# Kernel optimization log

Hardware: AMD Instinct MI355X
Metric: run time of the kernel (lower is better)

The kernel has to match this reference:

```python
import jax, jax.numpy as jnp
import numpy as np

N_NODES = 50000
SEQ_LEN = 32
N_TOKENS = 100000
EMB_DIM = 128          # in_feats / 2
IN_FEATS = 256
N_HIDDEN = 256
N_CLASSES = 40
N_EDGES = 800000
PAD_IX = 0


def setup_inputs() -> dict:
    key = jax.random.key(0)
    k1, k2, k3, k4, k5, k6 = jax.random.split(key, 6)
    features = jax.random.randint(k1, (N_NODES, SEQ_LEN), 0, N_TOKENS, dtype=jnp.int32)
    src = jax.random.randint(k2, (N_EDGES,), 0, N_NODES, dtype=jnp.int32)
    dst = jax.random.randint(k3, (N_EDGES,), 0, N_NODES, dtype=jnp.int32)
    emb_table = jax.random.normal(k4, (N_TOKENS, EMB_DIM), dtype=jnp.float32) * 0.02
    W1 = jax.random.normal(k5, (IN_FEATS, N_HIDDEN), dtype=jnp.float32) * 0.02
    b1 = jnp.zeros((N_HIDDEN,), dtype=jnp.float32)
    W2 = jax.random.normal(k6, (N_HIDDEN, N_CLASSES), dtype=jnp.float32) * 0.02
    b2 = jnp.zeros((N_CLASSES,), dtype=jnp.float32)
    return {"features": features, "src": src, "dst": dst,
            "emb_table": emb_table, "W1": W1, "b1": b1, "W2": W2, "b2": b2}


def _apply_embs(features, emb_table):
    # padding_idx row contributes zeros (nn.Embedding padding_idx semantics)
    emb = emb_table.at[PAD_IX].set(0.0)
    h = emb[features]                                    # [N, L, D]
    seq_len = jnp.sum(features != PAD_IX, axis=1)        # [N]
    seq_len = jnp.maximum(seq_len, 1)[:, None].astype(h.dtype)
    h1 = h.sum(axis=1) / seq_len                         # masked mean
    h2 = h.max(axis=1)                                   # max pool (pads are 0)
    return jnp.concatenate((h1, h2), axis=1)             # [N, 2D]


def _graph_conv(h, src, dst, norm_s, norm_d, W, b):
    # DGL GraphConv, norm='both': out = D_in^{-1/2} A D_out^{-1/2} h W + b
    hw = h @ W                                           # transform first (smaller msgs)
    m = (hw * norm_s[:, None])[src]                      # gather messages [E, F]
    agg = jax.ops.segment_sum(m, dst, num_segments=N_NODES)
    return agg * norm_d[:, None] + b


def reference(features, src, dst, emb_table, W1, b1, W2, b2):
    ones_e = jnp.ones((src.shape[0],), dtype=jnp.float32)
    deg_out = jnp.maximum(jax.ops.segment_sum(ones_e, src, num_segments=N_NODES), 1.0)
    deg_in = jnp.maximum(jax.ops.segment_sum(ones_e, dst, num_segments=N_NODES), 1.0)
    norm_s = deg_out ** -0.5
    norm_d = deg_in ** -0.5

    h = _apply_embs(features, emb_table)                 # [N, in_feats]
    h = jax.nn.relu(_graph_conv(h, src, dst, norm_s, norm_d, W1, b1))
    # dropout is identity in eval mode
    h = _graph_conv(h, src, dst, norm_s, norm_d, W2, b2)
    return h                                             # [N, n_classes]
```

## Files before the change

### kernel.cpp

```cpp
#include <hip/hip_runtime.h>
#include <math.h>

#define N_NODES 50000
#define SEQ_LEN 32
#define EMB_DIM 128
#define IN_FEATS 256
#define N_HIDDEN 256
#define N_CLASSES 40
#define N_EDGES 800000
#define N_TOKENS 100000

#define SLOT 64
#define NBIN 196
#define BINCAP 4608
#define EPB 4000

typedef short short8 __attribute__((ext_vector_type(8)));
typedef float f32x4 __attribute__((ext_vector_type(4)));

__device__ __forceinline__ unsigned short f2bf(float x) {
  unsigned int u = __float_as_uint(x);
  unsigned int r = (u + 0x7FFFu + ((u >> 16) & 1u)) >> 16;
  return (unsigned short)r;
}
__device__ __forceinline__ float bf2f(unsigned short s) {
  return __uint_as_float((unsigned int)s << 16);
}
__device__ __forceinline__ unsigned int pack2bf(float a, float b) {
  return (unsigned int)f2bf(a) | ((unsigned int)f2bf(b) << 16);
}

__global__ __launch_bounds__(256) void k_pre(const int* __restrict__ src,
                                             const int* __restrict__ dst,
                                             int* __restrict__ gcntD,
                                             int* __restrict__ gcntS,
                                             unsigned int* __restrict__ dbin,
                                             unsigned char* __restrict__ sbin,
                                             const float* __restrict__ emb,
                                             unsigned short* __restrict__ emb_b,
                                             const float* __restrict__ W1,
                                             unsigned short* __restrict__ Wp1,
                                             const float* __restrict__ W2,
                                             unsigned short* __restrict__ Wp2) {
  __shared__ int cntD[NBIN], cntS[NBIN], baseD[NBIN], baseS[NBIN];
  int b = blockIdx.x, tid = threadIdx.x;
  if (b < 200) {
    if (tid < NBIN) { cntD[tid] = 0; cntS[tid] = 0; }
    __syncthreads();
    int e0 = b * EPB;
    for (int j = tid; j < EPB; j += 256) {
      int d = dst[e0 + j], s = src[e0 + j];
      atomicAdd(&cntD[d >> 8], 1);
      atomicAdd(&cntS[s >> 8], 1);
    }
    __syncthreads();
    if (tid < NBIN) {
      baseD[tid] = atomicAdd(&gcntD[tid], cntD[tid]);
      baseS[tid] = atomicAdd(&gcntS[tid], cntS[tid]);
      cntD[tid] = 0;
      cntS[tid] = 0;
    }
    __syncthreads();
    for (int j = tid; j < EPB; j += 256) {
      int d = dst[e0 + j], s = src[e0 + j];
      int bd = d >> 8, bs = s >> 8;
      int od = atomicAdd(&cntD[bd], 1);
      int pd = baseD[bd] + od;
      if (pd < BINCAP) dbin[(size_t)bd * BINCAP + pd] = ((unsigned int)s << 8) | (unsigned int)(d & 255);
      int os = atomicAdd(&cntS[bs], 1);
      int ps = baseS[bs] + os;
      if (ps < BINCAP) sbin[(size_t)bs * BINCAP + ps] = (unsigned char)(s & 255);
    }
  } else if (b < 200 + 2048) {
    const int total = N_TOKENS * EMB_DIM / 4;
    for (int i = (b - 200) * 256 + tid; i < total; i += 2048 * 256) {
      float4 v = ((const float4*)emb)[i];
      ushort4 o;
      o.x = f2bf(v.x); o.y = f2bf(v.y); o.z = f2bf(v.z); o.w = f2bf(v.w);
      ((ushort4*)emb_b)[i] = o;
    }
  } else if (b < 200 + 2048 + 32) {
    int g = (b - 2248) * 256 + tid;
    int lane = g & 63, jb = (g >> 6) & 15, kt = g >> 10;
    int col = jb * 16 + (lane & 15);
    int kbase = kt * 32 + (lane >> 4) * 8;
    unsigned short* o = Wp1 + (size_t)g * 8;
    #pragma unroll
    for (int e = 0; e < 8; ++e) o[e] = f2bf(W1[(size_t)(kbase + e) * N_HIDDEN + col]);
  } else {
    int g = (b - 2280) * 256 + tid;
    if (g < 8 * 3 * 64) {
      int lane = g & 63, jb = (g >> 6) % 3, kt = g / (3 * 64);
      int col = jb * 16 + (lane & 15);
      int kbase = kt * 32 + (lane >> 4) * 8;
      unsigned short* o = Wp2 + (size_t)g * 8;
      #pragma unroll
      for (int e = 0; e < 8; ++e)
        o[e] = (col < N_CLASSES) ? f2bf(W2[(size_t)(kbase + e) * N_CLASSES + col]) : (unsigned short)0;
    }
  }
}

__global__ __launch_bounds__(256) void k_graph2(const unsigned int* __restrict__ dbin,
                                                const int* __restrict__ gcntD,
                                                const unsigned char* __restrict__ sbin,
                                                const int* __restrict__ gcntS,
                                                int* __restrict__ cursor,
                                                int* __restrict__ csr_pad,
                                                float* __restrict__ norm_s,
                                                float* __restrict__ norm_d) {
  __shared__ int cntD[256], cntS[256];
  int tid = threadIdx.x, b = blockIdx.x;
  cntD[tid] = 0; cntS[tid] = 0;
  __syncthreads();
  int n = min(gcntD[b], BINCAP);
  const unsigned int* bb = dbin + (size_t)b * BINCAP;
  for (int j = tid; j < n; j += 256) {
    unsigned int e = bb[j];
    int lo = e & 255;
    int slot = atomicAdd(&cntD[lo], 1);
    if (slot < SLOT) csr_pad[(size_t)(b * 256 + lo) * SLOT + slot] = (int)(e >> 8);
  }
  int ns = min(gcntS[b], BINCAP);
  const unsigned char* sb = sbin + (size_t)b * BINCAP;
  for (int j = tid; j < ns; j += 256) atomicAdd(&cntS[sb[j]], 1);
  __syncthreads();
  int node = b * 256 + tid;
  if (node < N_NODES) {
    cursor[node] = min(cntD[tid], SLOT);
    norm_d[node] = 1.0f / sqrtf((float)max(cntD[tid], 1));
    norm_s[node] = 1.0f / sqrtf((float)max(cntS[tid], 1));
  }
}

__global__ __launch_bounds__(512) void k_emb_mm1(const int* __restrict__ feats,
                                                 const uint4* __restrict__ rows4,
                                                 const unsigned short* __restrict__ Wp,
                                                 const float* __restrict__ norm_s,
                                                 unsigned short* __restrict__ out) {
  __shared__ unsigned short sA[64 * 256];
  int tid = threadIdx.x;
  int w = tid >> 6, lane = tid & 63;
  int r0 = blockIdx.x * 64;
  int lq = lane & 15, qg = lane >> 4, laneL = lane & 31;

  #pragma unroll
  for (int n = 0; n < 8; ++n) {
    int r = w * 8 + n;
    int node = r0 + r;
    int tok0 = 0;
    if (node < N_NODES) tok0 = feats[(size_t)node * SEQ_LEN + laneL];
    unsigned long long m = __ballot(tok0 != 0);
    int cnt = (int)__popcll(m & 0xFFFFFFFFull);
    float inv = 1.0f / (float)max(cnt, 1);

    float s0 = 0.f, s1 = 0.f, s2 = 0.f, s3 = 0.f, s4 = 0.f, s5 = 0.f, s6 = 0.f, s7 = 0.f;
    float m0 = 0.f, m1 = 0.f, m2 = 0.f, m3 = 0.f, m4 = 0.f, m5 = 0.f, m6 = 0.f, m7 = 0.f;
    bool first = true;
    #pragma unroll
    for (int t = 0; t < 8; ++t) {
      int tok = __shfl(tok0, t * 4 + qg);
      uint4 v = make_uint4(0u, 0u, 0u, 0u);
      if (tok) v = rows4[(size_t)tok * 16 + lq];
      float f0 = bf2f((unsigned short)(v.x & 0xFFFF)), f1 = bf2f((unsigned short)(v.x >> 16));
      float f2 = bf2f((unsigned short)(v.y & 0xFFFF)), f3 = bf2f((unsigned short)(v.y >> 16));
      float f4 = bf2f((unsigned short)(v.z & 0xFFFF)), f5 = bf2f((unsigned short)(v.z >> 16));
      float f6 = bf2f((unsigned short)(v.w & 0xFFFF)), f7 = bf2f((unsigned short)(v.w >> 16));
      s0 += f0; s1 += f1; s2 += f2; s3 += f3; s4 += f4; s5 += f5; s6 += f6; s7 += f7;
      if (first) { m0 = f0; m1 = f1; m2 = f2; m3 = f3; m4 = f4; m5 = f5; m6 = f6; m7 = f7; first = false; }
      else {
        m0 = fmaxf(m0, f0); m1 = fmaxf(m1, f1); m2 = fmaxf(m2, f2); m3 = fmaxf(m3, f3);
        m4 = fmaxf(m4, f4); m5 = fmaxf(m5, f5); m6 = fmaxf(m6, f6); m7 = fmaxf(m7, f7);
      }
    }
    #pragma unroll
    for (int mask = 16; mask <= 32; mask <<= 1) {
      s0 += __shfl_xor(s0, mask); s1 += __shfl_xor(s1, mask);
      s2 += __shfl_xor(s2, mask); s3 += __shfl_xor(s3, mask);
      s4 += __shfl_xor(s4, mask); s5 += __shfl_xor(s5, mask);
      s6 += __shfl_xor(s6, mask); s7 += __shfl_xor(s7, mask);
      m0 = fmaxf(m0, __shfl_xor(m0, mask)); m1 = fmaxf(m1, __shfl_xor(m1, mask));
      m2 = fmaxf(m2, __shfl_xor(m2, mask)); m3 = fmaxf(m3, __shfl_xor(m3, mask));
      m4 = fmaxf(m4, __shfl_xor(m4, mask)); m5 = fmaxf(m5, __shfl_xor(m5, mask));
      m6 = fmaxf(m6, __shfl_xor(m6, mask)); m7 = fmaxf(m7, __shfl_xor(m7, mask));
    }
    if (qg == 0) {
      int kb1 = lq, kb2 = 16 + lq;
      *(uint4*)&sA[r * 256 + ((kb1 ^ (r & 7)) << 3)] =
          make_uint4(pack2bf(s0 * inv, s1 * inv), pack2bf(s2 * inv, s3 * inv),
                     pack2bf(s4 * inv, s5 * inv), pack2bf(s6 * inv, s7 * inv));
      *(uint4*)&sA[r * 256 + ((kb2 ^ (r & 7)) << 3)] =
          make_uint4(pack2bf(m0, m1), pack2bf(m2, m3), pack2bf(m4, m5), pack2bf(m6, m7));
    }
  }
  __syncthreads();

  const short8* W8 = (const short8*)Wp;
  f32x4 acc[4][2];
  #pragma unroll
  for (int i = 0; i < 4; ++i) { acc[i][0] = (f32x4){0.f,0.f,0.f,0.f}; acc[i][1] = (f32x4){0.f,0.f,0.f,0.f}; }

  #pragma unroll
  for (int kt = 0; kt < 8; ++kt) {
    short8 a[4];
    int kb = kt * 4 + (lane >> 4);
    #pragma unroll
    for (int ri = 0; ri < 4; ++ri) {
      int r = ri * 16 + (lane & 15);
      a[ri] = *(const short8*)&sA[r * 256 + ((kb ^ (r & 7)) << 3)];
    }
    short8 b0 = W8[(kt * 16 + w * 2 + 0) * 64 + lane];
    short8 b1 = W8[(kt * 16 + w * 2 + 1) * 64 + lane];
    #pragma unroll
    for (int ri = 0; ri < 4; ++ri) {
      acc[ri][0] = __builtin_amdgcn_mfma_f32_16x16x32_bf16(a[ri], b0, acc[ri][0], 0, 0, 0);
      acc[ri][1] = __builtin_amdgcn_mfma_f32_16x16x32_bf16(a[ri], b1, acc[ri][1], 0, 0, 0);
    }
  }

  #pragma unroll
  for (int ri = 0; ri < 4; ++ri) {
    #pragma unroll
    for (int rr = 0; rr < 4; ++rr) {
      int row = r0 + ri * 16 + (lane >> 4) * 4 + rr;
      if (row < N_NODES) {
        float ns = norm_s[row];
        #pragma unroll
        for (int jb = 0; jb < 2; ++jb) {
          int col = w * 32 + jb * 16 + (lane & 15);
          out[(size_t)row * 256 + col] = f2bf(acc[ri][jb][rr] * ns);
        }
      }
    }
  }
}

__global__ __launch_bounds__(256) void k_agg1(const uint4* __restrict__ rows4,
                                              const int* __restrict__ cursor,
                                              const int* __restrict__ csr_pad,
                                              const float* __restrict__ norm_d,
                                              const float* __restrict__ b1,
                                              uint4* __restrict__ out4) {
  int tid = threadIdx.x;
  int w = tid >> 6, lane = tid & 63;
  int node = blockIdx.x * 4 + w;
  int cnt = __builtin_amdgcn_readfirstlane(cursor[node]);
  const int* csr = csr_pad + (size_t)node * SLOT;
  int half = lane >> 5, lq = lane & 31;

  float a0 = 0.f, a1 = 0.f, a2 = 0.f, a3 = 0.f, a4 = 0.f, a5 = 0.f, a6 = 0.f, a7 = 0.f;
  int e = 0;
  for (; e + 8 <= cnt; e += 8) {
    int s0 = csr[e + 0 + half], s1 = csr[e + 2 + half];
    int s2 = csr[e + 4 + half], s3 = csr[e + 6 + half];
    uint4 v0 = rows4[(size_t)s0 * 32 + lq];
    uint4 v1 = rows4[(size_t)s1 * 32 + lq];
    uint4 v2 = rows4[(size_t)s2 * 32 + lq];
    uint4 v3 = rows4[(size_t)s3 * 32 + lq];
    #pragma unroll
    for (int i = 0; i < 4; ++i) {
      uint4 v = (i == 0) ? v0 : (i == 1) ? v1 : (i == 2) ? v2 : v3;
      a0 += bf2f((unsigned short)(v.x & 0xFFFF)); a1 += bf2f((unsigned short)(v.x >> 16));
      a2 += bf2f((unsigned short)(v.y & 0xFFFF)); a3 += bf2f((unsigned short)(v.y >> 16));
      a4 += bf2f((unsigned short)(v.z & 0xFFFF)); a5 += bf2f((unsigned short)(v.z >> 16));
      a6 += bf2f((unsigned short)(v.w & 0xFFFF)); a7 += bf2f((unsigned short)(v.w >> 16));
    }
  }
  for (; e + 2 <= cnt; e += 2) {
    int s = csr[e + half];
    uint4 v = rows4[(size_t)s * 32 + lq];
    a0 += bf2f((unsigned short)(v.x & 0xFFFF)); a1 += bf2f((unsigned short)(v.x >> 16));
    a2 += bf2f((unsigned short)(v.y & 0xFFFF)); a3 += bf2f((unsigned short)(v.y >> 16));
    a4 += bf2f((unsigned short)(v.z & 0xFFFF)); a5 += bf2f((unsigned short)(v.z >> 16));
    a6 += bf2f((unsigned short)(v.w & 0xFFFF)); a7 += bf2f((unsigned short)(v.w >> 16));
  }
  if (e < cnt) {
    uint4 v = make_uint4(0u, 0u, 0u, 0u);
    if (half == 0) v = rows4[(size_t)csr[e] * 32 + lq];
    a0 += bf2f((unsigned short)(v.x & 0xFFFF)); a1 += bf2f((unsigned short)(v.x >> 16));
    a2 += bf2f((unsigned short)(v.y & 0xFFFF)); a3 += bf2f((unsigned short)(v.y >> 16));
    a4 += bf2f((unsigned short)(v.z & 0xFFFF)); a5 += bf2f((unsigned short)(v.z >> 16));
    a6 += bf2f((unsigned short)(v.w & 0xFFFF)); a7 += bf2f((unsigned short)(v.w >> 16));
  }
  a0 += __shfl_xor(a0, 32); a1 += __shfl_xor(a1, 32);
  a2 += __shfl_xor(a2, 32); a3 += __shfl_xor(a3, 32);
  a4 += __shfl_xor(a4, 32); a5 += __shfl_xor(a5, 32);
  a6 += __shfl_xor(a6, 32); a7 += __shfl_xor(a7, 32);

  if (half == 0) {
    float nd = norm_d[node];
    float4 bb0 = *(const float4*)&b1[8 * lq];
    float4 bb1 = *(const float4*)&b1[8 * lq + 4];
    float o0 = fmaxf(a0 * nd + bb0.x, 0.f), o1 = fmaxf(a1 * nd + bb0.y, 0.f);
    float o2 = fmaxf(a2 * nd + bb0.z, 0.f), o3 = fmaxf(a3 * nd + bb0.w, 0.f);
    float o4 = fmaxf(a4 * nd + bb1.x, 0.f), o5 = fmaxf(a5 * nd + bb1.y, 0.f);
    float o6 = fmaxf(a6 * nd + bb1.z, 0.f), o7 = fmaxf(a7 * nd + bb1.w, 0.f);
    out4[(size_t)node * 32 + lq] = make_uint4(pack2bf(o0, o1), pack2bf(o2, o3),
                                              pack2bf(o4, o5), pack2bf(o6, o7));
  }
}

__global__ __launch_bounds__(256) void k_mm2(const unsigned short* __restrict__ h2b,
                                             const unsigned short* __restrict__ Wp,
                                             const float* __restrict__ norm_s,
                                             unsigned short* __restrict__ out) {
  __shared__ unsigned short sA[64 * 256];
  int tid = threadIdx.x;
  int r0 = blockIdx.x * 64;
  #pragma unroll
  for (int it = 0; it < 8; ++it) {
    int idx = it * 256 + tid;
    int r = idx >> 5, kb = idx & 31;
    uint4 v = make_uint4(0, 0, 0, 0);
    int row = r0 + r;
    if (row < N_NODES) v = *(const uint4*)(h2b + (size_t)row * 256 + kb * 8);
    *(uint4*)&sA[r * 256 + ((kb ^ (r & 7)) << 3)] = v;
  }
  __syncthreads();

  int w = tid >> 6, lane = tid & 63;
  const short8* W8 = (const short8*)Wp;
  f32x4 acc[3];
  #pragma unroll
  for (int j = 0; j < 3; ++j) acc[j] = (f32x4){0.f, 0.f, 0.f, 0.f};

  #pragma unroll
  for (int kt = 0; kt < 8; ++kt) {
    int r = w * 16 + (lane & 15);
    int kb = kt * 4 + (lane >> 4);
    short8 a = *(const short8*)&sA[r * 256 + ((kb ^ (r & 7)) << 3)];
    #pragma unroll
    for (int jb = 0; jb < 3; ++jb) {
      short8 b = W8[(kt * 3 + jb) * 64 + lane];
      acc[jb] = __builtin_amdgcn_mfma_f32_16x16x32_bf16(a, b, acc[jb], 0, 0, 0);
    }
  }

  #pragma unroll
  for (int rr = 0; rr < 4; ++rr) {
    int row = r0 + w * 16 + (lane >> 4) * 4 + rr;
    if (row < N_NODES) {
      float ns = norm_s[row];
      #pragma unroll
      for (int jb = 0; jb < 3; ++jb) {
        int col = jb * 16 + (lane & 15);
        if (col < N_CLASSES) out[(size_t)row * N_CLASSES + col] = f2bf(acc[jb][rr] * ns);
      }
    }
  }
}

__global__ __launch_bounds__(256) void k_agg2(const uint2* __restrict__ rows2,
                                              const int* __restrict__ cursor,
                                              const int* __restrict__ csr_pad,
                                              const float* __restrict__ norm_d,
                                              const float* __restrict__ b2,
                                              float* __restrict__ out) {
  int tid = threadIdx.x;
  int w = tid >> 6, lane = tid & 63;
  int node = blockIdx.x * 4 + w;
  int slot = lane / 10, fl = lane % 10;
  int cnt = __builtin_amdgcn_readfirstlane(cursor[node]);
  const int* csr = csr_pad + (size_t)node * SLOT;

  float a0 = 0.f, a1 = 0.f, a2 = 0.f, a3 = 0.f;
  if (slot < 6) {
    for (int e = slot; e < cnt; e += 6) {
      int s = csr[e];
      uint2 v = rows2[(size_t)s * 10 + fl];
      a0 += bf2f((unsigned short)(v.x & 0xFFFF));
      a1 += bf2f((unsigned short)(v.x >> 16));
      a2 += bf2f((unsigned short)(v.y & 0xFFFF));
      a3 += bf2f((unsigned short)(v.y >> 16));
    }
  }
  float r10_0 = __shfl(a0, lane + 10), r10_1 = __shfl(a1, lane + 10), r10_2 = __shfl(a2, lane + 10), r10_3 = __shfl(a3, lane + 10);
  float r20_0 = __shfl(a0, lane + 20), r20_1 = __shfl(a1, lane + 20), r20_2 = __shfl(a2, lane + 20), r20_3 = __shfl(a3, lane + 20);
  float r30_0 = __shfl(a0, lane + 30), r30_1 = __shfl(a1, lane + 30), r30_2 = __shfl(a2, lane + 30), r30_3 = __shfl(a3, lane + 30);
  float r40_0 = __shfl(a0, lane + 40), r40_1 = __shfl(a1, lane + 40), r40_2 = __shfl(a2, lane + 40), r40_3 = __shfl(a3, lane + 40);
  float r50_0 = __shfl(a0, lane + 50), r50_1 = __shfl(a1, lane + 50), r50_2 = __shfl(a2, lane + 50), r50_3 = __shfl(a3, lane + 50);
  if (slot == 0) {
    a0 += r10_0 + r20_0 + r30_0 + r40_0 + r50_0;
    a1 += r10_1 + r20_1 + r30_1 + r40_1 + r50_1;
    a2 += r10_2 + r20_2 + r30_2 + r40_2 + r50_2;
    a3 += r10_3 + r20_3 + r30_3 + r40_3 + r50_3;
    float nd = norm_d[node];
    float4 bb = *(const float4*)&b2[4 * fl];
    float4 o = make_float4(a0 * nd + bb.x, a1 * nd + bb.y, a2 * nd + bb.z, a3 * nd + bb.w);
    *(float4*)&out[(size_t)node * N_CLASSES + 4 * fl] = o;
  }
}

extern "C" void kernel_launch(void* const* d_in, const int* in_sizes, int n_in,
                              void* d_out, int out_size, void* d_ws, size_t ws_size,
                              hipStream_t stream) {
  const int*   feats = (const int*)d_in[0];
  const int*   src   = (const int*)d_in[1];
  const int*   dst   = (const int*)d_in[2];
  const float* emb   = (const float*)d_in[3];
  const float* W1    = (const float*)d_in[4];
  const float* b1    = (const float*)d_in[5];
  const float* W2    = (const float*)d_in[6];
  const float* b2    = (const float*)d_in[7];
  float* out = (float*)d_out;

  char* base = (char*)d_ws;
  size_t off = 0;
  auto alloc = [&](size_t bytes) -> char* {
    char* p = base + off;
    off += (bytes + 255) & ~(size_t)255;
    return p;
  };
  unsigned short* hb      = (unsigned short*)alloc((size_t)N_NODES * N_HIDDEN * 2);
  unsigned short* msgb    = (unsigned short*)alloc((size_t)N_NODES * N_HIDDEN * 2);
  unsigned short* hw2b    = (unsigned short*)alloc((size_t)N_NODES * N_CLASSES * 2);
  unsigned short* emb_b   = (unsigned short*)alloc((size_t)N_TOKENS * EMB_DIM * 2);
  unsigned short* Wp1     = (unsigned short*)alloc((size_t)8 * 16 * 64 * 8 * 2);
  unsigned short* Wp2     = (unsigned short*)alloc((size_t)8 * 3 * 64 * 8 * 2);
  int*   gcnt    = (int*)alloc((size_t)512 * 4);
  int*   gcntD   = gcnt;
  int*   gcntS   = gcnt + 256;
  int*   cursor  = (int*)alloc((size_t)N_NODES * 4);
  float* norm_s  = (float*)alloc((size_t)N_NODES * 4);
  float* norm_d  = (float*)alloc((size_t)N_NODES * 4);
  unsigned int*  dbin = (unsigned int*)alloc((size_t)NBIN * BINCAP * 4);
  unsigned char* sbin = (unsigned char*)alloc((size_t)NBIN * BINCAP);
  int*   csr_pad = (int*)alloc((size_t)N_NODES * SLOT * 4);

  hipMemsetAsync(gcnt, 0, 512 * 4, stream);

  k_pre<<<200 + 2048 + 32 + 6, 256, 0, stream>>>(src, dst, gcntD, gcntS, dbin, sbin,
                                                 emb, emb_b, W1, Wp1, W2, Wp2);
  k_graph2<<<NBIN, 256, 0, stream>>>(dbin, gcntD, sbin, gcntS, cursor, csr_pad, norm_s, norm_d);

  int gemm_blocks = (N_NODES + 63) / 64;
  k_emb_mm1<<<gemm_blocks, 512, 0, stream>>>(feats, (const uint4*)emb_b, Wp1, norm_s, msgb);
  k_agg1<<<N_NODES / 4, 256, 0, stream>>>((const uint4*)msgb, cursor, csr_pad, norm_d, b1, (uint4*)hb);
  k_mm2<<<gemm_blocks, 256, 0, stream>>>(hb, Wp2, norm_s, hw2b);
  k_agg2<<<N_NODES / 4, 256, 0, stream>>>((const uint2*)hw2b, cursor, csr_pad, norm_d, b2, out);
}
```

Measured before the change: 212.3 us.

## Split embedding pooling from first GEMM and deepen aggregation unroll

Splits the fused embedding-pool plus first GEMM kernel into a standalone per-node embedding kernel writing bf16 features to global memory, and a separate 256-thread MFMA GEMM with 4x4 tiles per wave. This targets the poor latency hiding of the fused kernel, where few blocks each serially gathered embeddings for many rows. It also unrolls the first aggregation loop to 16 edges per iteration for more outstanding gathers. The cost is an extra write and read of the intermediate feature matrix plus one more launch.

```diff
diff --git a/kernel.cpp b/kernel.cpp
--- a/kernel.cpp
+++ b/kernel.cpp
@@ -29,6 +29,13 @@
 __device__ __forceinline__ unsigned int pack2bf(float a, float b) {
   return (unsigned int)f2bf(a) | ((unsigned int)f2bf(b) << 16);
 }
+
+#define ACC8(v) do { \
+  a[0] += bf2f((unsigned short)((v).x & 0xFFFF)); a[1] += bf2f((unsigned short)((v).x >> 16)); \
+  a[2] += bf2f((unsigned short)((v).y & 0xFFFF)); a[3] += bf2f((unsigned short)((v).y >> 16)); \
+  a[4] += bf2f((unsigned short)((v).z & 0xFFFF)); a[5] += bf2f((unsigned short)((v).z >> 16)); \
+  a[6] += bf2f((unsigned short)((v).w & 0xFFFF)); a[7] += bf2f((unsigned short)((v).w >> 16)); \
+} while (0)
 
 __global__ __launch_bounds__(256) void k_pre(const int* __restrict__ src,
                                              const int* __restrict__ dst,
@@ -133,89 +140,98 @@
   }
 }
 
-__global__ __launch_bounds__(512) void k_emb_mm1(const int* __restrict__ feats,
-                                                 const uint4* __restrict__ rows4,
-                                                 const unsigned short* __restrict__ Wp,
-                                                 const float* __restrict__ norm_s,
-                                                 unsigned short* __restrict__ out) {
+__global__ __launch_bounds__(256) void k_embed(const int* __restrict__ feats,
+                                               const uint4* __restrict__ rows4,
+                                               uint4* __restrict__ h4) {
+  int tid = threadIdx.x;
+  int w = tid >> 6, lane = tid & 63;
+  int node = blockIdx.x * 4 + w;
+  int lq = lane & 15, qg = lane >> 4;
+  int laneL = lane & 31;
+
+  int tok0 = feats[(size_t)node * SEQ_LEN + laneL];
+  unsigned long long m = __ballot(tok0 != 0);
+  int cnt = (int)__popcll(m & 0xFFFFFFFFull);
+  float inv = 1.0f / (float)max(cnt, 1);
+
+  float s0 = 0.f, s1 = 0.f, s2 = 0.f, s3 = 0.f, s4 = 0.f, s5 = 0.f, s6 = 0.f, s7 = 0.f;
+  float m0 = -INFINITY, m1 = -INFINITY, m2 = -INFINITY, m3 = -INFINITY;
+  float m4 = -INFINITY, m5 = -INFINITY, m6 = -INFINITY, m7 = -INFINITY;
+  #pragma unroll
+  for (int t = 0; t < 8; ++t) {
+    int tok = __shfl(tok0, t * 4 + qg);
+    uint4 v = make_uint4(0u, 0u, 0u, 0u);
+    if (tok) v = rows4[(size_t)tok * 16 + lq];
+    float f0 = bf2f((unsigned short)(v.x & 0xFFFF)), f1 = bf2f((unsigned short)(v.x >> 16));
+    float f2 = bf2f((unsigned short)(v.y & 0xFFFF)), f3 = bf2f((unsigned short)(v.y >> 16));
+    float f4 = bf2f((unsigned short)(v.z & 0xFFFF)), f5 = bf2f((unsigned short)(v.z >> 16));
+    float f6 = bf2f((unsigned short)(v.w & 0xFFFF)), f7 = bf2f((unsigned short)(v.w >> 16));
+    s0 += f0; s1 += f1; s2 += f2; s3 += f3; s4 += f4; s5 += f5; s6 += f6; s7 += f7;
+    m0 = fmaxf(m0, f0); m1 = fmaxf(m1, f1); m2 = fmaxf(m2, f2); m3 = fmaxf(m3, f3);
+    m4 = fmaxf(m4, f4); m5 = fmaxf(m5, f5); m6 = fmaxf(m6, f6); m7 = fmaxf(m7, f7);
+  }
+  #pragma unroll
+  for (int mask = 16; mask <= 32; mask <<= 1) {
+    s0 += __shfl_xor(s0, mask); s1 += __shfl_xor(s1, mask);
+    s2 += __shfl_xor(s2, mask); s3 += __shfl_xor(s3, mask);
+    s4 += __shfl_xor(s4, mask); s5 += __shfl_xor(s5, mask);
+    s6 += __shfl_xor(s6, mask); s7 += __shfl_xor(s7, mask);
+    m0 = fmaxf(m0, __shfl_xor(m0, mask)); m1 = fmaxf(m1, __shfl_xor(m1, mask));
+    m2 = fmaxf(m2, __shfl_xor(m2, mask)); m3 = fmaxf(m3, __shfl_xor(m3, mask));
+    m4 = fmaxf(m4, __shfl_xor(m4, mask)); m5 = fmaxf(m5, __shfl_xor(m5, mask));
+    m6 = fmaxf(m6, __shfl_xor(m6, mask)); m7 = fmaxf(m7, __shfl_xor(m7, mask));
+  }
+  if (qg == 0) {
+    uint4* hv = h4 + (size_t)node * 32;
+    hv[lq] = make_uint4(pack2bf(s0 * inv, s1 * inv), pack2bf(s2 * inv, s3 * inv),
+                        pack2bf(s4 * inv, s5 * inv), pack2bf(s6 * inv, s7 * inv));
+    hv[16 + lq] = make_uint4(pack2bf(m0, m1), pack2bf(m2, m3),
+                             pack2bf(m4, m5), pack2bf(m6, m7));
+  }
+}
+
+__global__ __launch_bounds__(256) void k_mm1(const unsigned short* __restrict__ hb,
+                                             const unsigned short* __restrict__ Wp,
+                                             const float* __restrict__ norm_s,
+                                             unsigned short* __restrict__ out) {
   __shared__ unsigned short sA[64 * 256];
   int tid = threadIdx.x;
+  int r0 = blockIdx.x * 64;
+  #pragma unroll
+  for (int it = 0; it < 8; ++it) {
+    int idx = it * 256 + tid;
+    int r = idx >> 5, kb = idx & 31;
+    uint4 v = make_uint4(0, 0, 0, 0);
+    int row = r0 + r;
+    if (row < N_NODES) v = *(const uint4*)(hb + (size_t)row * 256 + kb * 8);
+    *(uint4*)&sA[r * 256 + ((kb ^ (r & 7)) << 3)] = v;
+  }
+  __syncthreads();
+
   int w = tid >> 6, lane = tid & 63;
-  int r0 = blockIdx.x * 64;
-  int lq = lane & 15, qg = lane >> 4, laneL = lane & 31;
-
-  #pragma unroll
-  for (int n = 0; n < 8; ++n) {
-    int r = w * 8 + n;
-    int node = r0 + r;
-    int tok0 = 0;
-    if (node < N_NODES) tok0 = feats[(size_t)node * SEQ_LEN + laneL];
-    unsigned long long m = __ballot(tok0 != 0);
-    int cnt = (int)__popcll(m & 0xFFFFFFFFull);
-    float inv = 1.0f / (float)max(cnt, 1);
-
-    float s0 = 0.f, s1 = 0.f, s2 = 0.f, s3 = 0.f, s4 = 0.f, s5 = 0.f, s6 = 0.f, s7 = 0.f;
-    float m0 = 0.f, m1 = 0.f, m2 = 0.f, m3 = 0.f, m4 = 0.f, m5 = 0.f, m6 = 0.f, m7 = 0.f;
-    bool first = true;
-    #pragma unroll
-    for (int t = 0; t < 8; ++t) {
-      int tok = __shfl(tok0, t * 4 + qg);
-      uint4 v = make_uint4(0u, 0u, 0u, 0u);
-      if (tok) v = rows4[(size_t)tok * 16 + lq];
-      float f0 = bf2f((unsigned short)(v.x & 0xFFFF)), f1 = bf2f((unsigned short)(v.x >> 16));
-      float f2 = bf2f((unsigned short)(v.y & 0xFFFF)), f3 = bf2f((unsigned short)(v.y >> 16));
-      float f4 = bf2f((unsigned short)(v.z & 0xFFFF)), f5 = bf2f((unsigned short)(v.z >> 16));
-      float f6 = bf2f((unsigned short)(v.w & 0xFFFF)), f7 = bf2f((unsigned short)(v.w >> 16));
-      s0 += f0; s1 += f1; s2 += f2; s3 += f3; s4 += f4; s5 += f5; s6 += f6; s7 += f7;
-      if (first) { m0 = f0; m1 = f1; m2 = f2; m3 = f3; m4 = f4; m5 = f5; m6 = f6; m7 = f7; first = false; }
-      else {
-        m0 = fmaxf(m0, f0); m1 = fmaxf(m1, f1); m2 = fmaxf(m2, f2); m3 = fmaxf(m3, f3);
-        m4 = fmaxf(m4, f4); m5 = fmaxf(m5, f5); m6 = fmaxf(m6, f6); m7 = fmaxf(m7, f7);
-      }
-    }
-    #pragma unroll
-    for (int mask = 16; mask <= 32; mask <<= 1) {
-      s0 += __shfl_xor(s0, mask); s1 += __shfl_xor(s1, mask);
-      s2 += __shfl_xor(s2, mask); s3 += __shfl_xor(s3, mask);
-      s4 += __shfl_xor(s4, mask); s5 += __shfl_xor(s5, mask);
-      s6 += __shfl_xor(s6, mask); s7 += __shfl_xor(s7, mask);
-      m0 = fmaxf(m0, __shfl_xor(m0, mask)); m1 = fmaxf(m1, __shfl_xor(m1, mask));
-      m2 = fmaxf(m2, __shfl_xor(m2, mask)); m3 = fmaxf(m3, __shfl_xor(m3, mask));
-      m4 = fmaxf(m4, __shfl_xor(m4, mask)); m5 = fmaxf(m5, __shfl_xor(m5, mask));
-      m6 = fmaxf(m6, __shfl_xor(m6, mask)); m7 = fmaxf(m7, __shfl_xor(m7, mask));
-    }
-    if (qg == 0) {
-      int kb1 = lq, kb2 = 16 + lq;
-      *(uint4*)&sA[r * 256 + ((kb1 ^ (r & 7)) << 3)] =
-          make_uint4(pack2bf(s0 * inv, s1 * inv), pack2bf(s2 * inv, s3 * inv),
-                     pack2bf(s4 * inv, s5 * inv), pack2bf(s6 * inv, s7 * inv));
-      *(uint4*)&sA[r * 256 + ((kb2 ^ (r & 7)) << 3)] =
-          make_uint4(pack2bf(m0, m1), pack2bf(m2, m3), pack2bf(m4, m5), pack2bf(m6, m7));
-    }
-  }
-  __syncthreads();
-
   const short8* W8 = (const short8*)Wp;
-  f32x4 acc[4][2];
-  #pragma unroll
-  for (int i = 0; i < 4; ++i) { acc[i][0] = (f32x4){0.f,0.f,0.f,0.f}; acc[i][1] = (f32x4){0.f,0.f,0.f,0.f}; }
+  f32x4 acc[4][4];
+  #pragma unroll
+  for (int i = 0; i < 4; ++i)
+    #pragma unroll
+    for (int j = 0; j < 4; ++j) acc[i][j] = (f32x4){0.f, 0.f, 0.f, 0.f};
 
   #pragma unroll
   for (int kt = 0; kt < 8; ++kt) {
-    short8 a[4];
+    short8 a[4], b[4];
     int kb = kt * 4 + (lane >> 4);
     #pragma unroll
     for (int ri = 0; ri < 4; ++ri) {
       int r = ri * 16 + (lane & 15);
       a[ri] = *(const short8*)&sA[r * 256 + ((kb ^ (r & 7)) << 3)];
     }
-    short8 b0 = W8[(kt * 16 + w * 2 + 0) * 64 + lane];
-    short8 b1 = W8[(kt * 16 + w * 2 + 1) * 64 + lane];
-    #pragma unroll
-    for (int ri = 0; ri < 4; ++ri) {
-      acc[ri][0] = __builtin_amdgcn_mfma_f32_16x16x32_bf16(a[ri], b0, acc[ri][0], 0, 0, 0);
-      acc[ri][1] = __builtin_amdgcn_mfma_f32_16x16x32_bf16(a[ri], b1, acc[ri][1], 0, 0, 0);
-    }
+    #pragma unroll
+    for (int jb = 0; jb < 4; ++jb) b[jb] = W8[(kt * 16 + w * 4 + jb) * 64 + lane];
+    #pragma unroll
+    for (int ri = 0; ri < 4; ++ri)
+      #pragma unroll
+      for (int jb = 0; jb < 4; ++jb)
+        acc[ri][jb] = __builtin_amdgcn_mfma_f32_16x16x32_bf16(a[ri], b[jb], acc[ri][jb], 0, 0, 0);
   }
 
   #pragma unroll
@@ -226,8 +242,8 @@
       if (row < N_NODES) {
         float ns = norm_s[row];
         #pragma unroll
-        for (int jb = 0; jb < 2; ++jb) {
-          int col = w * 32 + jb * 16 + (lane & 15);
+        for (int jb = 0; jb < 4; ++jb) {
+          int col = w * 64 + jb * 16 + (lane & 15);
           out[(size_t)row * 256 + col] = f2bf(acc[ri][jb][rr] * ns);
         }
       }
@@ -248,53 +264,48 @@
   const int* csr = csr_pad + (size_t)node * SLOT;
   int half = lane >> 5, lq = lane & 31;
 
-  float a0 = 0.f, a1 = 0.f, a2 = 0.f, a3 = 0.f, a4 = 0.f, a5 = 0.f, a6 = 0.f, a7 = 0.f;
+  float a[8] = {0.f, 0.f, 0.f, 0.f, 0.f, 0.f, 0.f, 0.f};
   int e = 0;
+  for (; e + 16 <= cnt; e += 16) {
+    int s[8];
+    uint4 v[8];
+    #pragma unroll
+    for (int i = 0; i < 8; ++i) s[i] = csr[e + 2 * i + half];
+    #pragma unroll
+    for (int i = 0; i < 8; ++i) v[i] = rows4[(size_t)s[i] * 32 + lq];
+    #pragma unroll
+    for (int i = 0; i < 8; ++i) ACC8(v[i]);
+  }
   for (; e + 8 <= cnt; e += 8) {
-    int s0 = csr[e + 0 + half], s1 = csr[e + 2 + half];
-    int s2 = csr[e + 4 + half], s3 = csr[e + 6 + half];
-    uint4 v0 = rows4[(size_t)s0 * 32 + lq];
-    uint4 v1 = rows4[(size_t)s1 * 32 + lq];
-    uint4 v2 = rows4[(size_t)s2 * 32 + lq];
-    uint4 v3 = rows4[(size_t)s3 * 32 + lq];
-    #pragma unroll
-    for (int i = 0; i < 4; ++i) {
-      uint4 v = (i == 0) ? v0 : (i == 1) ? v1 : (i == 2) ? v2 : v3;
-      a0 += bf2f((unsigned short)(v.x & 0xFFFF)); a1 += bf2f((unsigned short)(v.x >> 16));
-      a2 += bf2f((unsigned short)(v.y & 0xFFFF)); a3 += bf2f((unsigned short)(v.y >> 16));
-      a4 += bf2f((unsigned short)(v.z & 0xFFFF)); a5 += bf2f((unsigned short)(v.z >> 16));
-      a6 += bf2f((unsigned short)(v.w & 0xFFFF)); a7 += bf2f((unsigned short)(v.w >> 16));
-    }
+    int s[4];
+    uint4 v[4];
+    #pragma unroll
+    for (int i = 0; i < 4; ++i) s[i] = csr[e + 2 * i + half];
+    #pragma unroll
+    for (int i = 0; i < 4; ++i) v[i] = rows4[(size_t)s[i] * 32 + lq];
+    #pragma unroll
+    for (int i = 0; i < 4; ++i) ACC8(v[i]);
   }
   for (; e + 2 <= cnt; e += 2) {
-    int s = csr[e + half];
-    uint4 v = rows4[(size_t)s * 32 + lq];
-    a0 += bf2f((unsigned short)(v.x & 0xFFFF)); a1 += bf2f((unsigned short)(v.x >> 16));
-    a2 += bf2f((unsigned short)(v.y & 0xFFFF)); a3 += bf2f((unsigned short)(v.y >> 16));
-    a4 += bf2f((unsigned short)(v.z & 0xFFFF)); a5 += bf2f((unsigned short)(v.z >> 16));
-    a6 += bf2f((unsigned short)(v.w & 0xFFFF)); a7 += bf2f((unsigned short)(v.w >> 16));
+    uint4 v = rows4[(size_t)csr[e + half] * 32 + lq];
+    ACC8(v);
   }
   if (e < cnt) {
     uint4 v = make_uint4(0u, 0u, 0u, 0u);
     if (half == 0) v = rows4[(size_t)csr[e] * 32 + lq];
-    a0 += bf2f((unsigned short)(v.x & 0xFFFF)); a1 += bf2f((unsigned short)(v.x >> 16));
-    a2 += bf2f((unsigned short)(v.y & 0xFFFF)); a3 += bf2f((unsigned short)(v.y >> 16));
-    a4 += bf2f((unsigned short)(v.z & 0xFFFF)); a5 += bf2f((unsigned short)(v.z >> 16));
-    a6 += bf2f((unsigned short)(v.w & 0xFFFF)); a7 += bf2f((unsigned short)(v.w >> 16));
-  }
-  a0 += __shfl_xor(a0, 32); a1 += __shfl_xor(a1, 32);
-  a2 += __shfl_xor(a2, 32); a3 += __shfl_xor(a3, 32);
-  a4 += __shfl_xor(a4, 32); a5 += __shfl_xor(a5, 32);
-  a6 += __shfl_xor(a6, 32); a7 += __shfl_xor(a7, 32);
+    ACC8(v);
+  }
+  #pragma unroll
+  for (int i = 0; i < 8; ++i) a[i] += __shfl_xor(a[i], 32);
 
   if (half == 0) {
     float nd = norm_d[node];
     float4 bb0 = *(const float4*)&b1[8 * lq];
     float4 bb1 = *(const float4*)&b1[8 * lq + 4];
-    float o0 = fmaxf(a0 * nd + bb0.x, 0.f), o1 = fmaxf(a1 * nd + bb0.y, 0.f);
-    float o2 = fmaxf(a2 * nd + bb0.z, 0.f), o3 = fmaxf(a3 * nd + bb0.w, 0.f);
-    float o4 = fmaxf(a4 * nd + bb1.x, 0.f), o5 = fmaxf(a5 * nd + bb1.y, 0.f);
-    float o6 = fmaxf(a6 * nd + bb1.z, 0.f), o7 = fmaxf(a7 * nd + bb1.w, 0.f);
+    float o0 = fmaxf(a[0] * nd + bb0.x, 0.f), o1 = fmaxf(a[1] * nd + bb0.y, 0.f);
+    float o2 = fmaxf(a[2] * nd + bb0.z, 0.f), o3 = fmaxf(a[3] * nd + bb0.w, 0.f);
+    float o4 = fmaxf(a[4] * nd + bb1.x, 0.f), o5 = fmaxf(a[5] * nd + bb1.y, 0.f);
+    float o6 = fmaxf(a[6] * nd + bb1.z, 0.f), o7 = fmaxf(a[7] * nd + bb1.w, 0.f);
     out4[(size_t)node * 32 + lq] = make_uint4(pack2bf(o0, o1), pack2bf(o2, o3),
                                               pack2bf(o4, o5), pack2bf(o6, o7));
   }
@@ -411,7 +422,7 @@
     off += (bytes + 255) & ~(size_t)255;
     return p;
   };
-  unsigned short* hb      = (unsigned short*)alloc((size_t)N_NODES * N_HIDDEN * 2);
+  unsigned short* hb      = (unsigned short*)alloc((size_t)N_NODES * IN_FEATS * 2);
   unsigned short* msgb    = (unsigned short*)alloc((size_t)N_NODES * N_HIDDEN * 2);
   unsigned short* hw2b    = (unsigned short*)alloc((size_t)N_NODES * N_CLASSES * 2);
   unsigned short* emb_b   = (unsigned short*)alloc((size_t)N_TOKENS * EMB_DIM * 2);
@@ -434,7 +445,8 @@
   k_graph2<<<NBIN, 256, 0, stream>>>(dbin, gcntD, sbin, gcntS, cursor, csr_pad, norm_s, norm_d);
 
   int gemm_blocks = (N_NODES + 63) / 64;
-  k_emb_mm1<<<gemm_blocks, 512, 0, stream>>>(feats, (const uint4*)emb_b, Wp1, norm_s, msgb);
+  k_embed<<<N_NODES / 4, 256, 0, stream>>>(feats, (const uint4*)emb_b, (uint4*)hb);
+  k_mm1<<<gemm_blocks, 256, 0, stream>>>(hb, Wp1, norm_s, msgb);
   k_agg1<<<N_NODES / 4, 256, 0, stream>>>((const uint4*)msgb, cursor, csr_pad, norm_d, b1, (uint4*)hb);
   k_mm2<<<gemm_blocks, 256, 0, stream>>>(hb, Wp2, norm_s, hw2b);
   k_agg2<<<N_NODES / 4, 256, 0, stream>>>((const uint2*)hw2b, cursor, csr_pad, norm_d, b2, out);
```

New measurement: 214.4 us. Within noise of the previous version (+1.0%).
